# Performance work log

Hardware: AMD Instinct MI355X
Metric: run time of the kernel (lower is better)

The kernel has to match this reference:

```python
import jax, jax.numpy as jnp
import numpy as np

S = 2048      # sequence length
D = 2048      # d_model
H = 16        # n_heads
E = 128       # d_head


def setup_inputs() -> dict:
    key = jax.random.key(0)
    kx, kw = jax.random.split(key)
    x = jax.random.normal(kx, (S, D), dtype=jnp.float32)
    # xavier_normal for fan_in=D, fan_out=3*E per head
    std = float(np.sqrt(2.0 / (D + 3 * E)))
    w_qkv = jax.random.normal(kw, (H, D, 3 * E), dtype=jnp.float32) * std
    return {"x": x, "w_qkv": w_qkv}


def reference(x, w_qkv):
    # qkv: [h, s, 3e]
    qkv = jnp.einsum('sd,hde->hse', x, w_qkv)
    q, k, v = jnp.split(qkv, 3, axis=-1)            # each [h, s, e]
    scores = jnp.einsum('hse,hte->hst', q, k) / jnp.sqrt(jnp.asarray(E, x.dtype))
    attn = jax.nn.softmax(scores, axis=-1)          # [h, s, t]
    out = jnp.einsum('hst,hte->hse', attn, v)       # [h, s, e]
    # concat heads: [s, h*e]
    return out.transpose(1, 0, 2).reshape(x.shape[0], -1)
```

## Files before the change

### kernel.cpp

```cpp
#include <hip/hip_runtime.h>

#define SEQ 2048
#define DMODEL 2048
#define NHEAD 16
#define EHEAD 128
#define NE3 384

using short8 = __attribute__((ext_vector_type(8))) short;
using f32x4  = __attribute__((ext_vector_type(4))) float;
using f32x16 = __attribute__((ext_vector_type(16))) float;
using uint4v = __attribute__((ext_vector_type(4))) unsigned int;
using uint2v = __attribute__((ext_vector_type(2))) unsigned int;

__device__ __forceinline__ unsigned short f32_to_bf16(float f) {
    unsigned int u = __float_as_uint(f);
    unsigned int rounding = 0x7fffu + ((u >> 16) & 1u);
    u += rounding;
    return (unsigned short)(u >> 16);
}

__device__ __forceinline__ void async_load16(const void* g, void* l) {
    __builtin_amdgcn_global_load_lds(
        (const __attribute__((address_space(1))) unsigned int*)g,
        (__attribute__((address_space(3))) unsigned int*)l, 16, 0, 0);
}

__global__ void prep_kernel(const float* __restrict__ x, unsigned short* __restrict__ xb,
                            const float* __restrict__ w, unsigned short* __restrict__ wT) {
    __shared__ float tile[64][65];
    const int bid = blockIdx.x;
    if (bid < 4096) {
        int i = (bid * blockDim.x + threadIdx.x) * 4;
        float4 v = *(const float4*)(x + i);
        ushort4 o = make_ushort4(f32_to_bf16(v.x), f32_to_bf16(v.y), f32_to_bf16(v.z), f32_to_bf16(v.w));
        *(ushort4*)(xb + i) = o;
        return;
    }
    const int b = bid - 4096;
    const int h  = b / 192;
    const int r6 = b % 192;
    const int n0 = (r6 / 32) * 64;
    const int d0 = (r6 % 32) * 64;
    int t = threadIdx.x;
    int rr = t >> 4;
    int cc = (t & 15) * 4;
#pragma unroll
    for (int i = 0; i < 4; i++) {
        float4 v = *(const float4*)&w[(size_t)(h * DMODEL + d0 + rr + i * 16) * NE3 + n0 + cc];
        tile[rr + i * 16][cc + 0] = v.x;
        tile[rr + i * 16][cc + 1] = v.y;
        tile[rr + i * 16][cc + 2] = v.z;
        tile[rr + i * 16][cc + 3] = v.w;
    }
    __syncthreads();
#pragma unroll
    for (int i = 0; i < 4; i++) {
        int n = rr + i * 16;
        ushort4 o;
        o.x = f32_to_bf16(tile[cc + 0][n]);
        o.y = f32_to_bf16(tile[cc + 1][n]);
        o.z = f32_to_bf16(tile[cc + 2][n]);
        o.w = f32_to_bf16(tile[cc + 3][n]);
        *(ushort4*)&wT[(size_t)(h * NE3 + n0 + n) * DMODEL + d0 + cc] = o;
    }
}

template <int B, bool STAGE, int VM, bool RDNEXT>
__device__ __forceinline__ void qkv_kstep(
        unsigned short* lds, f32x4 (&acc)[4][6],
        short8 (&aC)[4], short8 (&b0C)[3], short8 (&b1C)[3],
        short8 (&aN)[4], short8 (&b0N)[3], short8 (&b1N)[3],
        const unsigned short*& p0, const unsigned short*& p1,
        const unsigned short*& p2, const unsigned short*& p3,
        const int d0, const int d1, const int d2, const int d3,
        const int aoff, const int boff) {
    constexpr int NXT = ((B + 1) & 3) * 16384;
    constexpr int DST = ((B + 3) & 3) * 16384;

    if constexpr (STAGE) {
        async_load16(p0, lds + DST + d0);
        async_load16(p1, lds + DST + d1);
        async_load16(p2, lds + DST + d2);
        async_load16(p3, lds + DST + d3);
    }
    p0 += 32; p1 += 32; p2 += 32; p3 += 32;
    if constexpr (VM == 8)      asm volatile("s_waitcnt vmcnt(8)");
    else if constexpr (VM == 4) asm volatile("s_waitcnt vmcnt(4)");
    else if constexpr (VM == 0) asm volatile("s_waitcnt vmcnt(0)");
    asm volatile("s_waitcnt lgkmcnt(0)");
    __builtin_amdgcn_s_barrier();
    if constexpr (RDNEXT) {
#pragma unroll
        for (int mf = 0; mf < 4; ++mf) aN[mf]  = *(const short8*)(lds + NXT + aoff + mf * 512);
#pragma unroll
        for (int nf = 0; nf < 3; ++nf) b0N[nf] = *(const short8*)(lds + NXT + boff + nf * 512);
#pragma unroll
        for (int nf = 0; nf < 3; ++nf) b1N[nf] = *(const short8*)(lds + NXT + boff + (3 + nf) * 512);
    }
    __builtin_amdgcn_s_setprio(1);
#pragma unroll
    for (int mf = 0; mf < 4; ++mf)
#pragma unroll
        for (int nf = 0; nf < 3; ++nf)
            acc[mf][nf] = __builtin_amdgcn_mfma_f32_16x16x32_bf16(aC[mf], b0C[nf], acc[mf][nf], 0, 0, 0);
#pragma unroll
    for (int mf = 0; mf < 4; ++mf)
#pragma unroll
        for (int nf = 0; nf < 3; ++nf)
            acc[mf][3 + nf] = __builtin_amdgcn_mfma_f32_16x16x32_bf16(aC[mf], b1C[nf], acc[mf][3 + nf], 0, 0, 0);
    __builtin_amdgcn_s_setprio(0);
}

__global__ __launch_bounds__(512, 2) void qkv_gemm384(
        const unsigned short* __restrict__ A,
        const unsigned short* __restrict__ Bm,
        unsigned short* __restrict__ Q,
        unsigned short* __restrict__ Kb,
        unsigned short* __restrict__ Vt) {
    extern __shared__ __attribute__((aligned(16))) unsigned short lds[];
    const int mb = blockIdx.x, nb = blockIdx.y;
    const int tid = threadIdx.x;
    const int wave = tid >> 6, lane = tid & 63;
    const int r = lane & 15, q = lane >> 4;
    const int wm = wave >> 2, wn = wave & 3;

    const int rrm  = (tid >> 2) & 15;
    const int kg   = ((tid & 3) ^ ((rrm >> 1) & 3)) * 8;
    const int rowA = ((tid >> 6) << 4) + rrm;
    const unsigned short* p0 = A  + (size_t)(mb * 128 + rowA) * DMODEL + kg;
    const unsigned short* p1 = Bm + (size_t)(nb * 384 + rowA) * DMODEL + kg;
    const unsigned short* p2 = p1 + (size_t)128 * DMODEL;
    const unsigned short* p3 = p1 + (size_t)256 * DMODEL;
    const int d0 = wave * 512;
    const int d1 = 4096 + wave * 512;
    const int d2 = 8192 + wave * 512;
    const int d3 = 12288 + wave * 512;

#pragma unroll
    for (int t = 0; t < 3; ++t) {
        async_load16(p0 + t * 32, lds + t * 16384 + d0);
        async_load16(p1 + t * 32, lds + t * 16384 + d1);
        async_load16(p2 + t * 32, lds + t * 16384 + d2);
        async_load16(p3 + t * 32, lds + t * 16384 + d3);
    }
    p0 += 96; p1 += 96; p2 += 96; p3 += 96;

    const int qs = q ^ ((r >> 1) & 3);
    const int aoff = wm * 2048 + r * 32 + qs * 8;
    const int boff = 4096 + wn * 3072 + r * 32 + qs * 8;

    f32x4 acc[4][6] = {};
    asm volatile("s_waitcnt vmcnt(8)");
    __builtin_amdgcn_s_barrier();

    short8 aA[4], b0A[3], b1A[3], aB[4], b0B[3], b1B[3];
#pragma unroll
    for (int mf = 0; mf < 4; ++mf) aA[mf]  = *(const short8*)(lds + aoff + mf * 512);
#pragma unroll
    for (int nf = 0; nf < 3; ++nf) b0A[nf] = *(const short8*)(lds + boff + nf * 512);
#pragma unroll
    for (int nf = 0; nf < 3; ++nf) b1A[nf] = *(const short8*)(lds + boff + (3 + nf) * 512);

    for (int i = 0; i < 15; ++i) {
        qkv_kstep<0, true, 8, true>(lds, acc, aA, b0A, b1A, aB, b0B, b1B, p0, p1, p2, p3, d0, d1, d2, d3, aoff, boff);
        qkv_kstep<1, true, 8, true>(lds, acc, aB, b0B, b1B, aA, b0A, b1A, p0, p1, p2, p3, d0, d1, d2, d3, aoff, boff);
        qkv_kstep<2, true, 8, true>(lds, acc, aA, b0A, b1A, aB, b0B, b1B, p0, p1, p2, p3, d0, d1, d2, d3, aoff, boff);
        qkv_kstep<3, true, 8, true>(lds, acc, aB, b0B, b1B, aA, b0A, b1A, p0, p1, p2, p3, d0, d1, d2, d3, aoff, boff);
    }
    qkv_kstep<0, true,  8, true >(lds, acc, aA, b0A, b1A, aB, b0B, b1B, p0, p1, p2, p3, d0, d1, d2, d3, aoff, boff);
    qkv_kstep<1, false, 4, true >(lds, acc, aB, b0B, b1B, aA, b0A, b1A, p0, p1, p2, p3, d0, d1, d2, d3, aoff, boff);
    qkv_kstep<2, false, 0, true >(lds, acc, aA, b0A, b1A, aB, b0B, b1B, p0, p1, p2, p3, d0, d1, d2, d3, aoff, boff);
    qkv_kstep<3, false, -1, false>(lds, acc, aB, b0B, b1B, aA, b0A, b1A, p0, p1, p2, p3, d0, d1, d2, d3, aoff, boff);

    const int head = nb;
    const int mbase = mb * 128 + wm * 64;
#pragma unroll
    for (int nf = 0; nf < 6; ++nf) {
        const int cb = wn * 96 + nf * 16;
        const int sel = cb >> 7;
        const int e = (cb & 127) + r;
#pragma unroll
        for (int mf = 0; mf < 4; ++mf) {
            const int row0 = mbase + mf * 16 + q * 4;
            const f32x4 v = acc[mf][nf];
            if (sel == 2) {
                ushort4 o;
                o.x = f32_to_bf16(v[0]);
                o.y = f32_to_bf16(v[1]);
                o.z = f32_to_bf16(v[2]);
                o.w = f32_to_bf16(v[3]);
                *(ushort4*)&Vt[((size_t)head * EHEAD + e) * SEQ + row0] = o;
            } else {
                unsigned short* dst = sel ? Kb : Q;
#pragma unroll
                for (int reg = 0; reg < 4; ++reg)
                    dst[((size_t)head * SEQ + row0 + reg) * EHEAD + e] = f32_to_bf16(v[reg]);
            }
        }
    }
}

__global__ __launch_bounds__(512, 2) void flash_attn(
        const unsigned short* __restrict__ Qg,
        const unsigned short* __restrict__ Kg,
        const unsigned short* __restrict__ Vtg,
        float* __restrict__ out) {
    extern __shared__ __attribute__((aligned(16))) unsigned short lds[];
    unsigned short* sK0 = lds;
    unsigned short* sV0 = lds + 16384;

    const int tid = threadIdx.x;
    const int wave = tid >> 6, lane = tid & 63;
    const int l31 = lane & 31, q2 = lane >> 5;
    const int wm = wave >> 1, wn = wave & 1;
    const int b = blockIdx.x;
    const int h  = (b & 7) + ((b >> 7) << 3);
    const int m0 = ((b >> 3) & 15) * 128;

    const unsigned short* Qh  = Qg  + ((size_t)h * SEQ + m0) * EHEAD;
    const unsigned short* Kh0 = Kg  + (size_t)h * SEQ * EHEAD;
    const unsigned short* Vh  = Vtg + (size_t)h * EHEAD * SEQ;

    const int qkRow = lane >> 4;
    const int qkPos = lane & 15;
    const int vRow  = lane >> 3;
    const int vPos  = lane & 7;

    const unsigned short* gK[2];
    const unsigned short* gV[2];
#pragma unroll
    for (int c = 0; c < 2; c++) {
        int u = wave * 2 + c;
        int row = u * 4 + qkRow;
        int ch = qkPos ^ (row & 7);
        gK[c] = Kh0 + (size_t)row * EHEAD + ch * 8;
        int rv = u * 8 + vRow;
        int cv = vPos ^ (rv & 7);
        gV[c] = Vh + (size_t)rv * SEQ + cv * 8;
        async_load16(gK[c], sK0 + u * 512);
        async_load16(gV[c], sV0 + u * 512);
        gK[c] += 64 * EHEAD;
        gV[c] += 64;
    }

    short8 bq[8];
    {
        const unsigned short* qrow = Qh + (size_t)(wm * 32 + l31) * EHEAD;
#pragma unroll
        for (int kc = 0; kc < 8; kc++)
            bq[kc] = *(const short8*)(qrow + (kc * 2 + q2) * 8);
    }
    __syncthreads();

    const unsigned short* kp[8];
    const unsigned short* vp[8];
    const int rowA = wn * 32 + l31;
#pragma unroll
    for (int kc = 0; kc < 8; kc++)
        kp[kc] = sK0 + rowA * 128 + (((kc * 2 + q2) ^ (rowA & 7)) * 8);
#pragma unroll
    for (int et = 0; et < 4; et++)
#pragma unroll
        for (int kc2 = 0; kc2 < 2; kc2++) {
            int rowV = et * 32 + l31;
            int cch = wn * 4 + kc2 * 2 + q2;
            vp[et * 2 + kc2] = sV0 + rowV * 64 + ((cch ^ (rowV & 7)) * 8);
        }

    const float c1 = 0.12752405856f;
    f32x16 acc_o[4] = {};
    float l_acc0 = 0.f, l_acc1 = 0.f;

    auto body = [&](const int cur, const int nxt, bool pref) {
        if (pref) {
#pragma unroll
            for (int c = 0; c < 2; c++) {
                async_load16(gK[c], sK0 + nxt + (wave * 2 + c) * 512);
                gK[c] += 64 * EHEAD;
            }
#pragma unroll
            for (int c = 0; c < 2; c++) {
                async_load16(gV[c], sV0 + nxt + (wave * 2 + c) * 512);
                gV[c] += 64;
            }
        }

        f32x16 st0 = {}, st1 = {};
        __builtin_amdgcn_s_setprio(1);
#pragma unroll
        for (int kc = 0; kc < 8; kc += 2) {
            short8 ak0 = *(const short8*)(kp[kc] + cur);
            short8 ak1 = *(const short8*)(kp[kc + 1] + cur);
            st0 = __builtin_amdgcn_mfma_f32_32x32x16_bf16(ak0, bq[kc], st0, 0, 0, 0);
            st1 = __builtin_amdgcn_mfma_f32_32x32x16_bf16(ak1, bq[kc + 1], st1, 0, 0, 0);
        }
        __builtin_amdgcn_s_setprio(0);

        unsigned int pk[8];
#pragma unroll
        for (int t = 0; t < 8; t++) {
            float p0 = __builtin_amdgcn_exp2f((st0[2 * t] + st1[2 * t]) * c1);
            float p1 = __builtin_amdgcn_exp2f((st0[2 * t + 1] + st1[2 * t + 1]) * c1);
            l_acc0 += p0;
            l_acc1 += p1;
            unsigned int u0 = __float_as_uint(p0) + 0x8000u;
            unsigned int u1 = __float_as_uint(p1) + 0x8000u;
            pk[t] = __builtin_amdgcn_perm(u1, u0, 0x07060302u);
        }

        short8 fr[2];
#pragma unroll
        for (int kc2 = 0; kc2 < 2; kc2++) {
            unsigned int a0 = pk[kc2 * 4 + 0], a1 = pk[kc2 * 4 + 1];
            unsigned int a2 = pk[kc2 * 4 + 2], a3 = pk[kc2 * 4 + 3];
            uint2v r02 = __builtin_amdgcn_permlane32_swap(a0, a2, false, false);
            uint2v r13 = __builtin_amdgcn_permlane32_swap(a1, a3, false, false);
            uint4v t;
            t.x = r02[0];
            t.y = r13[0];
            t.z = r02[1];
            t.w = r13[1];
            fr[kc2] = __builtin_bit_cast(short8, t);
        }

        __builtin_amdgcn_s_setprio(1);
#pragma unroll
        for (int et = 0; et < 4; et++)
#pragma unroll
            for (int kc2 = 0; kc2 < 2; kc2++) {
                short8 bv = *(const short8*)(vp[et * 2 + kc2] + cur);
                acc_o[et] = __builtin_amdgcn_mfma_f32_32x32x16_bf16(fr[kc2], bv, acc_o[et], 0, 0, 0);
            }
        __builtin_amdgcn_s_setprio(0);
        __syncthreads();
    };

    for (int ip = 0; ip < SEQ / 128; ip++) {
        body(0, 8192, true);
        body(8192, 0, ip != SEQ / 128 - 1);
    }

    float l_acc = l_acc0 + l_acc1;
    l_acc += __shfl_xor(l_acc, 32);

    float* fl = (float*)lds;
#pragma unroll
    for (int et = 0; et < 4; et++) {
        if ((et >> 1) != wn) {
#pragma unroll
            for (int rg = 0; rg < 4; rg++) {
                f32x4 v;
                v[0] = acc_o[et][rg * 4 + 0];
                v[1] = acc_o[et][rg * 4 + 1];
                v[2] = acc_o[et][rg * 4 + 2];
                v[3] = acc_o[et][rg * 4 + 3];
                *(f32x4*)&fl[(size_t)(((wm * 4 + et) * 4 + rg) * 256) + lane * 4] = v;
            }
        }
    }
    fl[16384 + (wm * 2 + wn) * 32 + l31] = l_acc;
    __syncthreads();

    float invq[4][4];
#pragma unroll
    for (int rg = 0; rg < 4; rg++)
#pragma unroll
        for (int i = 0; i < 4; i++) {
            int qy = i + 4 * q2 + 8 * rg;
            float lt = fl[16384 + (wm * 2 + 0) * 32 + qy] + fl[16384 + (wm * 2 + 1) * 32 + qy];
            invq[rg][i] = 1.0f / lt;
        }

#pragma unroll
    for (int et = 0; et < 4; et++) {
        if ((et >> 1) == wn) {
#pragma unroll
            for (int rg = 0; rg < 4; rg++) {
                f32x4 v = *(const f32x4*)&fl[(size_t)(((wm * 4 + et) * 4 + rg) * 256) + lane * 4];
#pragma unroll
                for (int i = 0; i < 4; i++) {
                    int mrow = i + 4 * q2 + 8 * rg;
                    out[(size_t)(m0 + wm * 32 + mrow) * DMODEL + h * EHEAD + et * 32 + l31] =
                        (acc_o[et][rg * 4 + i] + v[i]) * invq[rg][i];
                }
            }
        }
    }
}

extern "C" void kernel_launch(void* const* d_in, const int* in_sizes, int n_in,
                              void* d_out, int out_size, void* d_ws, size_t ws_size,
                              hipStream_t stream) {
    const float* x = (const float*)d_in[0];
    const float* w = (const float*)d_in[1];
    float* out = (float*)d_out;

    char* ws = (char*)d_ws;
    unsigned short* xb = (unsigned short*)(ws);
    unsigned short* wT = (unsigned short*)(ws + 8388608);
    unsigned short* Q  = (unsigned short*)(ws + 33554432);
    unsigned short* Kb = (unsigned short*)(ws + 41943040);
    unsigned short* Vt = (unsigned short*)(ws + 50331648);

    static bool attr_set = false;
    if (!attr_set) {
        hipFuncSetAttribute((const void*)flash_attn,
                            hipFuncAttributeMaxDynamicSharedMemorySize, 66560);
        hipFuncSetAttribute((const void*)qkv_gemm384,
                            hipFuncAttributeMaxDynamicSharedMemorySize, 131072);
        attr_set = true;
    }

    prep_kernel<<<7168, 256, 0, stream>>>(x, xb, w, wT);
    qkv_gemm384<<<dim3(SEQ / 128, NHEAD), 512, 131072, stream>>>(xb, wT, Q, Kb, Vt);
    flash_attn<<<256, 512, 66560, stream>>>(Q, Kb, Vt, out);
}
```

Baseline: 190.5 us.

## Split QKV GEMM into 128x192 tiles with 4 waves and triple buffering

The QKV projection GEMM goes from 128x384 tiles with 8 waves and a 4-stage LDS ring to 128x192 tiles with 4 waves and a 3-stage ring. The grid doubles to 512 blocks and each block covers half a head's QKV columns. LDS per block drops from 128KB to 60KB, which is meant to allow more resident blocks per CU and better fill of the device. The cost is that each A tile is loaded twice and the prefetch depth is shallower.

Measured after the change: 199.7 us. +4.8%, slower.

```diff
diff --git a/kernel.cpp b/kernel.cpp
--- a/kernel.cpp
+++ b/kernel.cpp
@@ -72,20 +72,20 @@
         short8 (&aN)[4], short8 (&b0N)[3], short8 (&b1N)[3],
         const unsigned short*& p0, const unsigned short*& p1,
         const unsigned short*& p2, const unsigned short*& p3,
-        const int d0, const int d1, const int d2, const int d3,
-        const int aoff, const int boff) {
-    constexpr int NXT = ((B + 1) & 3) * 16384;
-    constexpr int DST = ((B + 3) & 3) * 16384;
+        const unsigned short*& p4,
+        const int wave, const int aoff, const int boff) {
+    constexpr int NXT = ((B + 1) % 3) * 10240;
+    constexpr int DST = ((B + 2) % 3) * 10240;
 
     if constexpr (STAGE) {
-        async_load16(p0, lds + DST + d0);
-        async_load16(p1, lds + DST + d1);
-        async_load16(p2, lds + DST + d2);
-        async_load16(p3, lds + DST + d3);
-    }
-    p0 += 32; p1 += 32; p2 += 32; p3 += 32;
-    if constexpr (VM == 8)      asm volatile("s_waitcnt vmcnt(8)");
-    else if constexpr (VM == 4) asm volatile("s_waitcnt vmcnt(4)");
+        async_load16(p0, lds + DST + wave * 512);
+        async_load16(p1, lds + DST + 2048 + wave * 512);
+        async_load16(p2, lds + DST + 4096 + wave * 512);
+        async_load16(p3, lds + DST + 6144 + wave * 512);
+        async_load16(p4, lds + DST + 8192 + wave * 512);
+    }
+    p0 += 32; p1 += 32; p2 += 32; p3 += 32; p4 += 32;
+    if constexpr (VM == 5)      asm volatile("s_waitcnt vmcnt(5)");
     else if constexpr (VM == 0) asm volatile("s_waitcnt vmcnt(0)");
     asm volatile("s_waitcnt lgkmcnt(0)");
     __builtin_amdgcn_s_barrier();
@@ -111,7 +111,7 @@
     __builtin_amdgcn_s_setprio(0);
 }
 
-__global__ __launch_bounds__(512, 2) void qkv_gemm384(
+__global__ __launch_bounds__(256, 2) void qkv_gemm192(
         const unsigned short* __restrict__ A,
         const unsigned short* __restrict__ Bm,
         unsigned short* __restrict__ Q,
@@ -122,35 +122,33 @@
     const int tid = threadIdx.x;
     const int wave = tid >> 6, lane = tid & 63;
     const int r = lane & 15, q = lane >> 4;
-    const int wm = wave >> 2, wn = wave & 3;
-
-    const int rrm  = (tid >> 2) & 15;
-    const int kg   = ((tid & 3) ^ ((rrm >> 1) & 3)) * 8;
-    const int rowA = ((tid >> 6) << 4) + rrm;
-    const unsigned short* p0 = A  + (size_t)(mb * 128 + rowA) * DMODEL + kg;
-    const unsigned short* p1 = Bm + (size_t)(nb * 384 + rowA) * DMODEL + kg;
-    const unsigned short* p2 = p1 + (size_t)128 * DMODEL;
-    const unsigned short* p3 = p1 + (size_t)256 * DMODEL;
-    const int d0 = wave * 512;
-    const int d1 = 4096 + wave * 512;
-    const int d2 = 8192 + wave * 512;
-    const int d3 = 12288 + wave * 512;
-
-#pragma unroll
-    for (int t = 0; t < 3; ++t) {
-        async_load16(p0 + t * 32, lds + t * 16384 + d0);
-        async_load16(p1 + t * 32, lds + t * 16384 + d1);
-        async_load16(p2 + t * 32, lds + t * 16384 + d2);
-        async_load16(p3 + t * 32, lds + t * 16384 + d3);
-    }
-    p0 += 96; p1 += 96; p2 += 96; p3 += 96;
+    const int wm = wave >> 1, wn = wave & 1;
+
+    const int rrm = (tid >> 2) & 15;
+    const int kg  = ((tid & 3) ^ ((rrm >> 1) & 3)) * 8;
+    const int row0g = (tid >> 6) * 16 + rrm;
+    const unsigned short* p0 = A  + (size_t)(mb * 128 + row0g) * DMODEL + kg;
+    const unsigned short* p1 = p0 + (size_t)64 * DMODEL;
+    const unsigned short* p2 = Bm + (size_t)(nb * 192 + row0g) * DMODEL + kg;
+    const unsigned short* p3 = p2 + (size_t)64 * DMODEL;
+    const unsigned short* p4 = p2 + (size_t)128 * DMODEL;
+
+#pragma unroll
+    for (int t = 0; t < 2; ++t) {
+        async_load16(p0 + t * 32, lds + t * 10240 + wave * 512);
+        async_load16(p1 + t * 32, lds + t * 10240 + 2048 + wave * 512);
+        async_load16(p2 + t * 32, lds + t * 10240 + 4096 + wave * 512);
+        async_load16(p3 + t * 32, lds + t * 10240 + 6144 + wave * 512);
+        async_load16(p4 + t * 32, lds + t * 10240 + 8192 + wave * 512);
+    }
+    p0 += 64; p1 += 64; p2 += 64; p3 += 64; p4 += 64;
 
     const int qs = q ^ ((r >> 1) & 3);
     const int aoff = wm * 2048 + r * 32 + qs * 8;
     const int boff = 4096 + wn * 3072 + r * 32 + qs * 8;
 
     f32x4 acc[4][6] = {};
-    asm volatile("s_waitcnt vmcnt(8)");
+    asm volatile("s_waitcnt vmcnt(5)");
     __builtin_amdgcn_s_barrier();
 
     short8 aA[4], b0A[3], b1A[3], aB[4], b0B[3], b1B[3];
@@ -161,22 +159,24 @@
 #pragma unroll
     for (int nf = 0; nf < 3; ++nf) b1A[nf] = *(const short8*)(lds + boff + (3 + nf) * 512);
 
-    for (int i = 0; i < 15; ++i) {
-        qkv_kstep<0, true, 8, true>(lds, acc, aA, b0A, b1A, aB, b0B, b1B, p0, p1, p2, p3, d0, d1, d2, d3, aoff, boff);
-        qkv_kstep<1, true, 8, true>(lds, acc, aB, b0B, b1B, aA, b0A, b1A, p0, p1, p2, p3, d0, d1, d2, d3, aoff, boff);
-        qkv_kstep<2, true, 8, true>(lds, acc, aA, b0A, b1A, aB, b0B, b1B, p0, p1, p2, p3, d0, d1, d2, d3, aoff, boff);
-        qkv_kstep<3, true, 8, true>(lds, acc, aB, b0B, b1B, aA, b0A, b1A, p0, p1, p2, p3, d0, d1, d2, d3, aoff, boff);
-    }
-    qkv_kstep<0, true,  8, true >(lds, acc, aA, b0A, b1A, aB, b0B, b1B, p0, p1, p2, p3, d0, d1, d2, d3, aoff, boff);
-    qkv_kstep<1, false, 4, true >(lds, acc, aB, b0B, b1B, aA, b0A, b1A, p0, p1, p2, p3, d0, d1, d2, d3, aoff, boff);
-    qkv_kstep<2, false, 0, true >(lds, acc, aA, b0A, b1A, aB, b0B, b1B, p0, p1, p2, p3, d0, d1, d2, d3, aoff, boff);
-    qkv_kstep<3, false, -1, false>(lds, acc, aB, b0B, b1B, aA, b0A, b1A, p0, p1, p2, p3, d0, d1, d2, d3, aoff, boff);
-
-    const int head = nb;
+    for (int i = 0; i < 10; ++i) {
+        qkv_kstep<0, true, 5, true>(lds, acc, aA, b0A, b1A, aB, b0B, b1B, p0, p1, p2, p3, p4, wave, aoff, boff);
+        qkv_kstep<1, true, 5, true>(lds, acc, aB, b0B, b1B, aA, b0A, b1A, p0, p1, p2, p3, p4, wave, aoff, boff);
+        qkv_kstep<2, true, 5, true>(lds, acc, aA, b0A, b1A, aB, b0B, b1B, p0, p1, p2, p3, p4, wave, aoff, boff);
+        qkv_kstep<0, true, 5, true>(lds, acc, aB, b0B, b1B, aA, b0A, b1A, p0, p1, p2, p3, p4, wave, aoff, boff);
+        qkv_kstep<1, true, 5, true>(lds, acc, aA, b0A, b1A, aB, b0B, b1B, p0, p1, p2, p3, p4, wave, aoff, boff);
+        qkv_kstep<2, true, 5, true>(lds, acc, aB, b0B, b1B, aA, b0A, b1A, p0, p1, p2, p3, p4, wave, aoff, boff);
+    }
+    qkv_kstep<0, true,  5, true >(lds, acc, aA, b0A, b1A, aB, b0B, b1B, p0, p1, p2, p3, p4, wave, aoff, boff);
+    qkv_kstep<1, true,  5, true >(lds, acc, aB, b0B, b1B, aA, b0A, b1A, p0, p1, p2, p3, p4, wave, aoff, boff);
+    qkv_kstep<2, false, 0, true >(lds, acc, aA, b0A, b1A, aB, b0B, b1B, p0, p1, p2, p3, p4, wave, aoff, boff);
+    qkv_kstep<0, false, -1, false>(lds, acc, aB, b0B, b1B, aA, b0A, b1A, p0, p1, p2, p3, p4, wave, aoff, boff);
+
+    const int head = nb >> 1;
     const int mbase = mb * 128 + wm * 64;
 #pragma unroll
     for (int nf = 0; nf < 6; ++nf) {
-        const int cb = wn * 96 + nf * 16;
+        const int cb = (nb & 1) * 192 + wn * 96 + nf * 16;
         const int sel = cb >> 7;
         const int e = (cb & 127) + r;
 #pragma unroll
@@ -406,12 +406,12 @@
     if (!attr_set) {
         hipFuncSetAttribute((const void*)flash_attn,
                             hipFuncAttributeMaxDynamicSharedMemorySize, 66560);
-        hipFuncSetAttribute((const void*)qkv_gemm384,
-                            hipFuncAttributeMaxDynamicSharedMemorySize, 131072);
+        hipFuncSetAttribute((const void*)qkv_gemm192,
+                            hipFuncAttributeMaxDynamicSharedMemorySize, 61440);
         attr_set = true;
     }
 
     prep_kernel<<<7168, 256, 0, stream>>>(x, xb, w, wT);
-    qkv_gemm384<<<dim3(SEQ / 128, NHEAD), 512, 131072, stream>>>(xb, wT, Q, Kb, Vt);
+    qkv_gemm192<<<dim3(SEQ / 128, NHEAD * 2), 256, 61440, stream>>>(xb, wT, Q, Kb, Vt);
     flash_attn<<<256, 512, 66560, stream>>>(Q, Kb, Vt, out);
 }
```
